# Kernel tuning notes

Hardware: AMD Instinct MI355X
Metric: run time of the kernel (lower is better)

The kernel has to match this reference:

```python
import jax, jax.numpy as jnp
import numpy as np

L, B, F, H, C = 1024, 8, 256, 8, 32  # seq, batch, feature_dim, heads, head_size
EPS = 1e-5


def setup_inputs() -> dict:
    key = jax.random.key(0)
    ks = jax.random.split(key, 12)
    s = 0.02
    f32 = jnp.float32
    return {
        "features": jax.random.normal(ks[0], (L, B, F), f32),
        "ln_g": jnp.ones((F,), f32),
        "ln_b": jnp.zeros((F,), f32),
        "Wq": jax.random.normal(ks[1], (F, H * C), f32) * s,
        "bq": jnp.zeros((H * C,), f32),
        "Wk": jax.random.normal(ks[2], (F, H * C), f32) * s,
        "bk": jnp.zeros((H * C,), f32),
        "Wv": jax.random.normal(ks[3], (F, H * C), f32) * s,
        "bv": jnp.zeros((H * C,), f32),
        "Wb": jax.random.normal(ks[4], (F, H), f32) * s,
        "bb": jnp.zeros((H,), f32),
        "Wg": jax.random.normal(ks[5], (F, H * C), f32) * s,
        "bg": jnp.zeros((H * C,), f32),
        "Wo": jax.random.normal(ks[6], (H * C, F), f32) * s,
        "bo": jnp.zeros((F,), f32),
    }


def _layernorm(x, g, b):
    mu = jnp.mean(x, axis=-1, keepdims=True)
    var = jnp.var(x, axis=-1, keepdims=True)
    return (x - mu) * jax.lax.rsqrt(var + EPS) * g + b


def reference(features, ln_g, ln_b, Wq, bq, Wk, bk, Wv, bv, Wb, bb, Wg, bg, Wo, bo):
    # features: (L, B, F) -- sequence-first layout (see einsum axis analysis)
    x = _layernorm(features, ln_g, ln_b)
    q = (x @ Wq + bq).reshape(L, B, H, C)  # (Lq, B, H, C)
    k = (x @ Wk + bk).reshape(L, B, H, C)  # (Lk, B, H, C)
    v = (x @ Wv + bv).reshape(L, B, H, C)
    bias = x @ Wb + bb                      # (Lk, B, H) per-key-position bias
    gate = jax.nn.sigmoid(x @ Wg + bg).reshape(L, B, H, C)

    sq_c = 1.0 / np.sqrt(C).astype(np.float32)
    # logits[q, b, k, h]
    logits = jnp.einsum('qbhc,kbhc->qbkh', q, k) * sq_c
    logits = logits + jnp.transpose(bias, (1, 0, 2))[None]  # (1, B, Lk, H)
    w = jax.nn.softmax(logits, axis=2)                      # softmax over keys
    attn = jnp.einsum('qbkh,kbhc->qbhc', w, v)              # (Lq, B, H, C)
    out = (attn * gate).reshape(L, B, H * C)
    return out @ Wo + bo                                    # (L, B, F)
```

## Files before the change

kernel.cpp:

```cpp
#include <hip/hip_runtime.h>
#include <math.h>

#define LQ 1024
#define BB 8
#define FF 256
#define HH 8
#define CC 32
#define MROWS (LQ*BB)
static constexpr float EPSV  = 1e-5f;
static constexpr float LOG2E = 1.4426950408889634f;
static constexpr float C1    = 0.17677669529663687f * 1.4426950408889634f;

typedef short  short8  __attribute__((ext_vector_type(8)));
typedef short  short4v __attribute__((ext_vector_type(4)));
typedef float  float4v __attribute__((ext_vector_type(4)));

__device__ inline unsigned short f2bf(float f) {
    unsigned int u = __builtin_bit_cast(unsigned int, f);
    u += 0x7FFFu + ((u >> 16) & 1u);
    return (unsigned short)(u >> 16);
}
__device__ inline float bf2f(unsigned short h) {
    unsigned int u = ((unsigned int)h) << 16;
    return __builtin_bit_cast(float, u);
}
__device__ inline unsigned int cvt_pk_bf16(float a, float b) {
    unsigned int r;
    asm("v_cvt_pk_bf16_f32 %0, %1, %2" : "=v"(r) : "v"(a), "v"(b));
    return r;
}
__device__ __forceinline__ void gl_lds16(const unsigned short* g, unsigned short* l) {
    __builtin_amdgcn_global_load_lds(
        (const __attribute__((address_space(1))) void*)g,
        (__attribute__((address_space(3))) void*)l, 16, 0, 0);
}

__global__ __launch_bounds__(256)
void prep_ln_kernel(const float* __restrict__ x, const float* __restrict__ g,
                    const float* __restrict__ bln,
                    const float* __restrict__ Wq, const float* __restrict__ Wk,
                    const float* __restrict__ Wv, const float* __restrict__ Wg,
                    const float* __restrict__ Wo, const float* __restrict__ Wb,
                    const float* __restrict__ bq, const float* __restrict__ bk,
                    const float* __restrict__ bv, const float* __restrict__ bg,
                    unsigned short* __restrict__ xb, unsigned short* __restrict__ wt,
                    unsigned short* __restrict__ wto,
                    float* __restrict__ bcomb, float* __restrict__ wbt) {
    int bid = blockIdx.x;
    if (bid < 2048) {
        int wid  = threadIdx.x >> 6;
        int lane = threadIdx.x & 63;
        int row  = bid * 4 + wid;
        float4 v = reinterpret_cast<const float4*>(x + (size_t)row * FF)[lane];
        float s  = v.x + v.y + v.z + v.w;
        float sq = v.x*v.x + v.y*v.y + v.z*v.z + v.w*v.w;
        #pragma unroll
        for (int m = 1; m < 64; m <<= 1) {
            s  += __shfl_xor(s,  m);
            sq += __shfl_xor(sq, m);
        }
        float mean = s * (1.0f / FF);
        float var  = sq * (1.0f / FF) - mean * mean;
        float rstd = rsqrtf(var + EPSV);
        float4 gg = reinterpret_cast<const float4*>(g)[lane];
        float4 bv4 = reinterpret_cast<const float4*>(bln)[lane];
        short4v o;
        o[0] = (short)f2bf((v.x - mean) * rstd * gg.x + bv4.x);
        o[1] = (short)f2bf((v.y - mean) * rstd * gg.y + bv4.y);
        o[2] = (short)f2bf((v.z - mean) * rstd * gg.z + bv4.z);
        o[3] = (short)f2bf((v.w - mean) * rstd * gg.w + bv4.w);
        *reinterpret_cast<short4v*>(xb + (size_t)row * FF + lane * 4) = o;
    } else if (bid < 2112) {
        int k0 = (bid - 2048) * 4;
        int nl = threadIdx.x;
        const float* Ws[5] = {Wq, Wk, Wv, Wg, Wo};
        #pragma unroll
        for (int sel = 0; sel < 5; ++sel) {
            const float* W = Ws[sel];
            short4v o;
            #pragma unroll
            for (int j = 0; j < 4; ++j)
                o[j] = (short)f2bf(W[(size_t)(k0 + j) * 256 + nl]);
            unsigned short* dst = (sel < 4)
                ? (wt + ((size_t)sel * 256 + nl) * 256 + k0)
                : (wto + (size_t)nl * 256 + k0);
            *reinterpret_cast<short4v*>(dst) = o;
        }
        if (k0 == 0) {
            bcomb[nl]       = bq[nl];
            bcomb[256 + nl] = bk[nl];
            bcomb[512 + nl] = bv[nl];
            bcomb[768 + nl] = bg[nl];
        }
    } else {
        int nl = threadIdx.x;
        #pragma unroll
        for (int hh = 0; hh < 8; ++hh)
            wbt[hh * 256 + nl] = Wb[(size_t)nl * 8 + hh];
    }
}

__global__ __launch_bounds__(256)
void qkvg_fused_kernel(const unsigned short* __restrict__ A,
                       const unsigned short* __restrict__ Bt,
                       const float* __restrict__ bcomb,
                       const float* __restrict__ wbt,
                       const float* __restrict__ bbv,
                       unsigned short* __restrict__ outq,
                       float* __restrict__ outb) {
    __shared__ unsigned short Asb[128 * 64];
    __shared__ unsigned short Bsb[128 * 64];
    int bid = blockIdx.x;
    int tid = threadIdx.x;

    if (bid >= 512) {
        int idx = (bid - 512) * 256 + tid;
        int row = idx >> 3, hh = idx & 7;
        const unsigned short* xr = A + (size_t)row * 256;
        const float* wr = wbt + hh * 256;
        float s = 0.f;
        #pragma unroll 4
        for (int i = 0; i < 32; ++i) {
            short8 x8 = *reinterpret_cast<const short8*>(xr + i * 8);
            float4 wa = *reinterpret_cast<const float4*>(wr + i * 8);
            float4 wb2 = *reinterpret_cast<const float4*>(wr + i * 8 + 4);
            s += bf2f((unsigned short)x8[0]) * wa.x + bf2f((unsigned short)x8[1]) * wa.y
               + bf2f((unsigned short)x8[2]) * wa.z + bf2f((unsigned short)x8[3]) * wa.w;
            s += bf2f((unsigned short)x8[4]) * wb2.x + bf2f((unsigned short)x8[5]) * wb2.y
               + bf2f((unsigned short)x8[6]) * wb2.z + bf2f((unsigned short)x8[7]) * wb2.w;
        }
        outb[idx] = s + bbv[hh];
        return;
    }

    int lane = tid & 63;
    int w    = tid >> 6;
    int wm   = w >> 1, wn = w & 1;
    int l15  = lane & 15, lg = lane >> 4;
    int bm   = (bid & 63) * 128;
    int bn   = (bid >> 6) * 128;

    float4v acc[4][4];
    #pragma unroll
    for (int i = 0; i < 4; ++i)
        #pragma unroll
        for (int j = 0; j < 4; ++j)
            acc[i][j] = (float4v){0.f, 0.f, 0.f, 0.f};

    for (int k0 = 0; k0 < 256; k0 += 64) {
        __syncthreads();
        #pragma unroll
        for (int j = 0; j < 4; ++j) {
            int c = w * 4 + j;
            int u = c * 64 + lane;
            int row = u >> 3, slot = u & 7;
            size_t gsw = (size_t)row * 256 + k0 + ((slot ^ (row & 7)) * 8);
            gl_lds16(A + (size_t)bm * 256 + gsw, Asb + c * 512);
            gl_lds16(Bt + (size_t)bn * 256 + gsw, Bsb + c * 512);
        }
        __syncthreads();
        #pragma unroll
        for (int kh = 0; kh < 2; ++kh) {
            int slot = kh * 4 + lg;
            short8 af[4], bf[4];
            #pragma unroll
            for (int mf = 0; mf < 4; ++mf) {
                int row = wm * 64 + mf * 16 + l15;
                af[mf] = *reinterpret_cast<const short8*>(
                    Asb + row * 64 + ((slot ^ (row & 7)) * 8));
            }
            #pragma unroll
            for (int nf = 0; nf < 4; ++nf) {
                int row = wn * 64 + nf * 16 + l15;
                bf[nf] = *reinterpret_cast<const short8*>(
                    Bsb + row * 64 + ((slot ^ (row & 7)) * 8));
            }
            #pragma unroll
            for (int mf = 0; mf < 4; ++mf)
                #pragma unroll
                for (int nf = 0; nf < 4; ++nf)
                    acc[mf][nf] = __builtin_amdgcn_mfma_f32_16x16x32_bf16(
                        bf[nf], af[mf], acc[mf][nf], 0, 0, 0);
        }
    }

    int sel = bn >> 8;
    unsigned short* outp = outq + (size_t)sel * MROWS * 256;
    #pragma unroll
    for (int mf = 0; mf < 4; ++mf) {
        int m = bm + wm * 64 + mf * 16 + l15;
        #pragma unroll
        for (int nf = 0; nf < 4; ++nf) {
            int nglob = bn + wn * 64 + nf * 16 + lg * 4;
            float4 b4 = *reinterpret_cast<const float4*>(bcomb + nglob);
            float v0 = acc[mf][nf][0] + b4.x;
            float v1 = acc[mf][nf][1] + b4.y;
            float v2 = acc[mf][nf][2] + b4.z;
            float v3 = acc[mf][nf][3] + b4.w;
            if (sel == 3) {
                v0 = 1.0f / (1.0f + __expf(-v0));
                v1 = 1.0f / (1.0f + __expf(-v1));
                v2 = 1.0f / (1.0f + __expf(-v2));
                v3 = 1.0f / (1.0f + __expf(-v3));
            }
            uint2 st;
            st.x = cvt_pk_bf16(v0, v1);
            st.y = cvt_pk_bf16(v2, v3);
            *reinterpret_cast<uint2*>(outp + (size_t)m * 256 + (nglob & 255)) = st;
        }
    }
}

__global__ __launch_bounds__(512)
void attn_mfma_kernel(const unsigned short* __restrict__ qkvg,
                      const float* __restrict__ biasp,
                      unsigned short* __restrict__ ag) {
    __shared__ unsigned short ksl[128][40];
    __shared__ unsigned short vt[32 * 128];
    __shared__ unsigned short ps[8][16 * 128];
    __shared__ float bias_s[128];
    const unsigned short* qb = qkvg;
    const unsigned short* kb = qkvg + (size_t)MROWS * 256;
    const unsigned short* vb = qkvg + (size_t)MROWS * 256 * 2;
    const unsigned short* gb = qkvg + (size_t)MROWS * 256 * 3;

    int tid  = threadIdx.x;
    int lane = tid & 63;
    int w    = tid >> 6;
    int l15  = lane & 15, lg = lane >> 4;
    int bh   = blockIdx.y;
    int b    = bh >> 3, h = bh & 7;
    int qrow0 = blockIdx.x * 128 + w * 16;

    int krow = tid >> 2, kc8 = (tid & 3) * 8;
    int cv = (tid & 7) * 4, kp = tid >> 3;

    short8 qf = *reinterpret_cast<const short8*>(
        qb + ((size_t)(qrow0 + l15) * 8 + b) * 256 + h * 32 + lg * 8);

    float lsum = 0.f;
    float4v oacc0 = {0.f, 0.f, 0.f, 0.f}, oacc1 = {0.f, 0.f, 0.f, 0.f};

    short8 kreg; short4v v0r, v1r; float breg = 0.f;
    {
        kreg = *reinterpret_cast<const short8*>(
            kb + ((size_t)krow * 8 + b) * 256 + h * 32 + kc8);
        const unsigned short* vp =
            vb + ((size_t)(2 * kp) * 8 + b) * 256 + h * 32 + cv;
        v0r = *reinterpret_cast<const short4v*>(vp);
        v1r = *reinterpret_cast<const short4v*>(vp + 8 * 256);
        if (tid < 128) breg = biasp[(size_t)tid * 64 + b * 8 + h] * LOG2E;
    }

    for (int c0 = 0; c0 < LQ; c0 += 128) {
        __syncthreads();
        *reinterpret_cast<short8*>(&ksl[krow][kc8]) = kreg;
        #pragma unroll
        for (int j = 0; j < 4; ++j) {
            int c = cv + j;
            unsigned int pk = (unsigned int)(unsigned short)v0r[j] |
                              ((unsigned int)(unsigned short)v1r[j] << 16);
            int slot = kp >> 2;
            int off  = c * 128 + ((slot ^ (c & 7)) * 8) + ((2 * kp) & 7);
            *reinterpret_cast<unsigned int*>(&vt[off]) = pk;
        }
        if (tid < 128) bias_s[tid] = breg;
        __syncthreads();
        int cn = c0 + 128;
        if (cn < LQ) {
            kreg = *reinterpret_cast<const short8*>(
                kb + ((size_t)(cn + krow) * 8 + b) * 256 + h * 32 + kc8);
            const unsigned short* vp =
                vb + ((size_t)(cn + 2 * kp) * 8 + b) * 256 + h * 32 + cv;
            v0r = *reinterpret_cast<const short4v*>(vp);
            v1r = *reinterpret_cast<const short4v*>(vp + 8 * 256);
            if (tid < 128) breg = biasp[(size_t)(cn + tid) * 64 + b * 8 + h] * LOG2E;
        }

        __builtin_amdgcn_s_setprio(1);
        float4v sc[8];
        #pragma unroll
        for (int kt = 0; kt < 8; ++kt) {
            short8 kf = *reinterpret_cast<const short8*>(&ksl[kt * 16 + l15][lg * 8]);
            sc[kt] = __builtin_amdgcn_mfma_f32_16x16x32_bf16(
                kf, qf, (float4v){0.f, 0.f, 0.f, 0.f}, 0, 0, 0);
        }
        __builtin_amdgcn_s_setprio(0);

        float psum = 0.f;
        #pragma unroll
        for (int kt = 0; kt < 8; ++kt) {
            float4v b4 = *reinterpret_cast<const float4v*>(&bias_s[kt * 16 + lg * 4]);
            float p0 = __builtin_amdgcn_exp2f(fmaf(sc[kt][0], C1, b4[0]));
            float p1 = __builtin_amdgcn_exp2f(fmaf(sc[kt][1], C1, b4[1]));
            float p2 = __builtin_amdgcn_exp2f(fmaf(sc[kt][2], C1, b4[2]));
            float p3 = __builtin_amdgcn_exp2f(fmaf(sc[kt][3], C1, b4[3]));
            psum += (p0 + p1) + (p2 + p3);
            uint2 pk;
            pk.x = cvt_pk_bf16(p0, p1);
            pk.y = cvt_pk_bf16(p2, p3);
            int slot = kt * 2 + (lg >> 1);
            int off  = l15 * 128 + ((slot ^ (l15 & 7)) * 8) + (lg & 1) * 4;
            *reinterpret_cast<uint2*>(&ps[w][off]) = pk;
        }
        psum += __shfl_xor(psum, 16);
        psum += __shfl_xor(psum, 32);
        lsum += psum;

        __builtin_amdgcn_s_setprio(1);
        #pragma unroll
        for (int kh = 0; kh < 4; ++kh) {
            int slot = kh * 4 + lg;
            short8 pf = *reinterpret_cast<const short8*>(
                &ps[w][l15 * 128 + ((slot ^ (l15 & 7)) * 8)]);
            int c0r = l15, c1r = 16 + l15;
            short8 vf0 = *reinterpret_cast<const short8*>(
                &vt[c0r * 128 + ((slot ^ (c0r & 7)) * 8)]);
            short8 vf1 = *reinterpret_cast<const short8*>(
                &vt[c1r * 128 + ((slot ^ (c1r & 7)) * 8)]);
            oacc0 = __builtin_amdgcn_mfma_f32_16x16x32_bf16(vf0, pf, oacc0, 0, 0, 0);
            oacc1 = __builtin_amdgcn_mfma_f32_16x16x32_bf16(vf1, pf, oacc1, 0, 0, 0);
        }
        __builtin_amdgcn_s_setprio(0);
    }

    float linv = 1.0f / lsum;
    size_t base = ((size_t)(qrow0 + l15) * 8 + b) * 256 + h * 32;
    #pragma unroll
    for (int ct = 0; ct < 2; ++ct) {
        int c0 = ct * 16 + lg * 4;
        float4v oa = ct ? oacc1 : oacc0;
        short4v g4 = *reinterpret_cast<const short4v*>(gb + base + c0);
        float v0 = oa[0] * linv * bf2f((unsigned short)g4[0]);
        float v1 = oa[1] * linv * bf2f((unsigned short)g4[1]);
        float v2 = oa[2] * linv * bf2f((unsigned short)g4[2]);
        float v3 = oa[3] * linv * bf2f((unsigned short)g4[3]);
        uint2 st;
        st.x = cvt_pk_bf16(v0, v1);
        st.y = cvt_pk_bf16(v2, v3);
        *reinterpret_cast<uint2*>(ag + base + c0) = st;
    }
}

__global__ __launch_bounds__(256)
void gemm_out_kernel(const unsigned short* __restrict__ A,
                     const unsigned short* __restrict__ Bt,
                     const float* __restrict__ bias,
                     float* __restrict__ Cout) {
    __shared__ unsigned short Asb[64 * 64];
    __shared__ unsigned short Bsb[128 * 64];
    int tid  = threadIdx.x;
    int lane = tid & 63;
    int w    = tid >> 6;
    int l15  = lane & 15, lg = lane >> 4;
    int bm   = blockIdx.x * 64;
    int bn   = blockIdx.y * 128;

    float4v acc[4][2];
    #pragma unroll
    for (int i = 0; i < 4; ++i)
        #pragma unroll
        for (int j = 0; j < 2; ++j)
            acc[i][j] = (float4v){0.f, 0.f, 0.f, 0.f};

    for (int k0 = 0; k0 < 256; k0 += 64) {
        __syncthreads();
        #pragma unroll
        for (int j = 0; j < 2; ++j) {
            int c = w * 2 + j;
            int u = c * 64 + lane;
            int row = u >> 3, slot = u & 7;
            gl_lds16(A + (size_t)(bm + row) * 256 + k0 + ((slot ^ (row & 7)) * 8),
                     Asb + c * 512);
        }
        #pragma unroll
        for (int j = 0; j < 4; ++j) {
            int c = w * 4 + j;
            int u = c * 64 + lane;
            int row = u >> 3, slot = u & 7;
            gl_lds16(Bt + (size_t)(bn + row) * 256 + k0 + ((slot ^ (row & 7)) * 8),
                     Bsb + c * 512);
        }
        __syncthreads();
        #pragma unroll
        for (int kh = 0; kh < 2; ++kh) {
            int slot = kh * 4 + lg;
            short8 af[4], bf[2];
            #pragma unroll
            for (int mf = 0; mf < 4; ++mf) {
                int row = mf * 16 + l15;
                af[mf] = *reinterpret_cast<const short8*>(
                    Asb + row * 64 + ((slot ^ (row & 7)) * 8));
            }
            #pragma unroll
            for (int nf = 0; nf < 2; ++nf) {
                int row = w * 32 + nf * 16 + l15;
                bf[nf] = *reinterpret_cast<const short8*>(
                    Bsb + row * 64 + ((slot ^ (row & 7)) * 8));
            }
            #pragma unroll
            for (int mf = 0; mf < 4; ++mf)
                #pragma unroll
                for (int nf = 0; nf < 2; ++nf)
                    acc[mf][nf] = __builtin_amdgcn_mfma_f32_16x16x32_bf16(
                        bf[nf], af[mf], acc[mf][nf], 0, 0, 0);
        }
    }
    #pragma unroll
    for (int mf = 0; mf < 4; ++mf) {
        int m = bm + mf * 16 + l15;
        #pragma unroll
        for (int nf = 0; nf < 2; ++nf) {
            int c0 = bn + w * 32 + nf * 16 + lg * 4;
            float4 b4 = *reinterpret_cast<const float4*>(bias + c0);
            float4 o;
            o.x = acc[mf][nf][0] + b4.x;
            o.y = acc[mf][nf][1] + b4.y;
            o.z = acc[mf][nf][2] + b4.z;
            o.w = acc[mf][nf][3] + b4.w;
            *reinterpret_cast<float4*>(Cout + (size_t)m * 256 + c0) = o;
        }
    }
}

extern "C" void kernel_launch(void* const* d_in, const int* in_sizes, int n_in,
                              void* d_out, int out_size, void* d_ws, size_t ws_size,
                              hipStream_t stream) {
    (void)in_sizes; (void)n_in; (void)out_size; (void)ws_size;
    const float* features = (const float*)d_in[0];
    const float* ln_g = (const float*)d_in[1];
    const float* ln_b = (const float*)d_in[2];
    const float* Wq = (const float*)d_in[3];
    const float* bq = (const float*)d_in[4];
    const float* Wk = (const float*)d_in[5];
    const float* bk = (const float*)d_in[6];
    const float* Wv = (const float*)d_in[7];
    const float* bv = (const float*)d_in[8];
    const float* Wb = (const float*)d_in[9];
    const float* bbv = (const float*)d_in[10];
    const float* Wg = (const float*)d_in[11];
    const float* bg = (const float*)d_in[12];
    const float* Wo = (const float*)d_in[13];
    const float* bo = (const float*)d_in[14];
    float* out = (float*)d_out;

    char* wsb = (char*)d_ws;
    unsigned short* xb    = (unsigned short*)(wsb);
    unsigned short* wt    = (unsigned short*)(wsb + 4194304);
    unsigned short* wto   = (unsigned short*)(wsb + 4718592);
    float*          bcomb = (float*)(wsb + 4849664);
    float*          wbt   = (float*)(wsb + 4853760);
    unsigned short* qkvg  = (unsigned short*)(wsb + 4861952);
    float*          biasb = (float*)(wsb + 21639168);
    unsigned short* agb   = (unsigned short*)(wsb + 21901312);

    prep_ln_kernel<<<dim3(2113), dim3(256), 0, stream>>>(
        features, ln_g, ln_b, Wq, Wk, Wv, Wg, Wo, Wb,
        bq, bk, bv, bg, xb, wt, wto, bcomb, wbt);
    qkvg_fused_kernel<<<dim3(768), dim3(256), 0, stream>>>(
        xb, wt, bcomb, wbt, bbv, qkvg, biasb);
    attn_mfma_kernel<<<dim3(8, 64), dim3(512), 0, stream>>>(
        qkvg, biasb, agb);
    gemm_out_kernel<<<dim3(128, 2), dim3(256), 0, stream>>>(
        agb, wto, bo, out);
}
```

Baseline: 59.38 us.

## Give each attention wave two query tiles and halve the block size

The attention kernel now runs 4 waves per block instead of 8, and each wave handles 32 query rows (two 16-row MFMA tiles). Each K and V fragment read from LDS is reused across both query tiles. Each 128-key chunk is split into two 64-key halves so the per-wave P scratch buffer stays small. The aim is fewer LDS reads per MFMA and less block-wide staging overhead, at the cost of more registers per thread and fewer waves available to hide latency.

```diff
diff --git a/kernel.cpp b/kernel.cpp
--- a/kernel.cpp
+++ b/kernel.cpp
@@ -211,13 +211,13 @@
     }
 }
 
-__global__ __launch_bounds__(512)
+__global__ __launch_bounds__(256)
 void attn_mfma_kernel(const unsigned short* __restrict__ qkvg,
                       const float* __restrict__ biasp,
                       unsigned short* __restrict__ ag) {
     __shared__ unsigned short ksl[128][40];
     __shared__ unsigned short vt[32 * 128];
-    __shared__ unsigned short ps[8][16 * 128];
+    __shared__ unsigned short ps[4][32 * 64];
     __shared__ float bias_s[128];
     const unsigned short* qb = qkvg;
     const unsigned short* kb = qkvg + (size_t)MROWS * 256;
@@ -230,115 +230,172 @@
     int l15  = lane & 15, lg = lane >> 4;
     int bh   = blockIdx.y;
     int b    = bh >> 3, h = bh & 7;
-    int qrow0 = blockIdx.x * 128 + w * 16;
-
-    int krow = tid >> 2, kc8 = (tid & 3) * 8;
-    int cv = (tid & 7) * 4, kp = tid >> 3;
-
-    short8 qf = *reinterpret_cast<const short8*>(
-        qb + ((size_t)(qrow0 + l15) * 8 + b) * 256 + h * 32 + lg * 8);
-
-    float lsum = 0.f;
-    float4v oacc0 = {0.f, 0.f, 0.f, 0.f}, oacc1 = {0.f, 0.f, 0.f, 0.f};
-
-    short8 kreg; short4v v0r, v1r; float breg = 0.f;
+    int qrow0 = blockIdx.x * 128 + w * 32;
+
+    int cv = (tid & 7) * 4, kp0 = tid >> 3;
+
+    short8 qf[2];
+    #pragma unroll
+    for (int qt = 0; qt < 2; ++qt)
+        qf[qt] = *reinterpret_cast<const short8*>(
+            qb + ((size_t)(qrow0 + qt * 16 + l15) * 8 + b) * 256 + h * 32 + lg * 8);
+
+    float lsum[2] = {0.f, 0.f};
+    float4v oacc[2][2];
+    #pragma unroll
+    for (int i = 0; i < 2; ++i)
+        #pragma unroll
+        for (int j = 0; j < 2; ++j) oacc[i][j] = (float4v){0.f, 0.f, 0.f, 0.f};
+
+    short8 kreg[2]; short4v v0r[2], v1r[2]; float breg = 0.f;
     {
-        kreg = *reinterpret_cast<const short8*>(
-            kb + ((size_t)krow * 8 + b) * 256 + h * 32 + kc8);
-        const unsigned short* vp =
-            vb + ((size_t)(2 * kp) * 8 + b) * 256 + h * 32 + cv;
-        v0r = *reinterpret_cast<const short4v*>(vp);
-        v1r = *reinterpret_cast<const short4v*>(vp + 8 * 256);
+        #pragma unroll
+        for (int j = 0; j < 2; ++j) {
+            int u = j * 256 + tid;
+            int row = u >> 2, slot = u & 3;
+            kreg[j] = *reinterpret_cast<const short8*>(
+                kb + ((size_t)row * 8 + b) * 256 + h * 32 + slot * 8);
+        }
+        #pragma unroll
+        for (int gI = 0; gI < 2; ++gI) {
+            const unsigned short* vp =
+                vb + ((size_t)(2 * kp0 + 64 * gI) * 8 + b) * 256 + h * 32 + cv;
+            v0r[gI] = *reinterpret_cast<const short4v*>(vp);
+            v1r[gI] = *reinterpret_cast<const short4v*>(vp + 8 * 256);
+        }
         if (tid < 128) breg = biasp[(size_t)tid * 64 + b * 8 + h] * LOG2E;
     }
 
     for (int c0 = 0; c0 < LQ; c0 += 128) {
         __syncthreads();
-        *reinterpret_cast<short8*>(&ksl[krow][kc8]) = kreg;
-        #pragma unroll
-        for (int j = 0; j < 4; ++j) {
-            int c = cv + j;
-            unsigned int pk = (unsigned int)(unsigned short)v0r[j] |
-                              ((unsigned int)(unsigned short)v1r[j] << 16);
+        #pragma unroll
+        for (int j = 0; j < 2; ++j) {
+            int u = j * 256 + tid;
+            int row = u >> 2, slot = u & 3;
+            *reinterpret_cast<short8*>(&ksl[row][slot * 8]) = kreg[j];
+        }
+        #pragma unroll
+        for (int gI = 0; gI < 2; ++gI) {
+            int kp = kp0 + 32 * gI;
             int slot = kp >> 2;
-            int off  = c * 128 + ((slot ^ (c & 7)) * 8) + ((2 * kp) & 7);
-            *reinterpret_cast<unsigned int*>(&vt[off]) = pk;
+            #pragma unroll
+            for (int j = 0; j < 4; ++j) {
+                int c = cv + j;
+                unsigned int pk = (unsigned int)(unsigned short)v0r[gI][j] |
+                                  ((unsigned int)(unsigned short)v1r[gI][j] << 16);
+                int off = c * 128 + ((slot ^ (c & 7)) * 8) + ((2 * kp0) & 7);
+                *reinterpret_cast<unsigned int*>(&vt[off]) = pk;
+            }
         }
         if (tid < 128) bias_s[tid] = breg;
         __syncthreads();
         int cn = c0 + 128;
         if (cn < LQ) {
-            kreg = *reinterpret_cast<const short8*>(
-                kb + ((size_t)(cn + krow) * 8 + b) * 256 + h * 32 + kc8);
-            const unsigned short* vp =
-                vb + ((size_t)(cn + 2 * kp) * 8 + b) * 256 + h * 32 + cv;
-            v0r = *reinterpret_cast<const short4v*>(vp);
-            v1r = *reinterpret_cast<const short4v*>(vp + 8 * 256);
+            #pragma unroll
+            for (int j = 0; j < 2; ++j) {
+                int u = j * 256 + tid;
+                int row = u >> 2, slot = u & 3;
+                kreg[j] = *reinterpret_cast<const short8*>(
+                    kb + ((size_t)(cn + row) * 8 + b) * 256 + h * 32 + slot * 8);
+            }
+            #pragma unroll
+            for (int gI = 0; gI < 2; ++gI) {
+                const unsigned short* vp =
+                    vb + ((size_t)(cn + 2 * kp0 + 64 * gI) * 8 + b) * 256 + h * 32 + cv;
+                v0r[gI] = *reinterpret_cast<const short4v*>(vp);
+                v1r[gI] = *reinterpret_cast<const short4v*>(vp + 8 * 256);
+            }
             if (tid < 128) breg = biasp[(size_t)(cn + tid) * 64 + b * 8 + h] * LOG2E;
         }
 
-        __builtin_amdgcn_s_setprio(1);
-        float4v sc[8];
-        #pragma unroll
-        for (int kt = 0; kt < 8; ++kt) {
-            short8 kf = *reinterpret_cast<const short8*>(&ksl[kt * 16 + l15][lg * 8]);
-            sc[kt] = __builtin_amdgcn_mfma_f32_16x16x32_bf16(
-                kf, qf, (float4v){0.f, 0.f, 0.f, 0.f}, 0, 0, 0);
-        }
-        __builtin_amdgcn_s_setprio(0);
-
-        float psum = 0.f;
-        #pragma unroll
-        for (int kt = 0; kt < 8; ++kt) {
-            float4v b4 = *reinterpret_cast<const float4v*>(&bias_s[kt * 16 + lg * 4]);
-            float p0 = __builtin_amdgcn_exp2f(fmaf(sc[kt][0], C1, b4[0]));
-            float p1 = __builtin_amdgcn_exp2f(fmaf(sc[kt][1], C1, b4[1]));
-            float p2 = __builtin_amdgcn_exp2f(fmaf(sc[kt][2], C1, b4[2]));
-            float p3 = __builtin_amdgcn_exp2f(fmaf(sc[kt][3], C1, b4[3]));
-            psum += (p0 + p1) + (p2 + p3);
-            uint2 pk;
-            pk.x = cvt_pk_bf16(p0, p1);
-            pk.y = cvt_pk_bf16(p2, p3);
-            int slot = kt * 2 + (lg >> 1);
-            int off  = l15 * 128 + ((slot ^ (l15 & 7)) * 8) + (lg & 1) * 4;
-            *reinterpret_cast<uint2*>(&ps[w][off]) = pk;
-        }
-        psum += __shfl_xor(psum, 16);
-        psum += __shfl_xor(psum, 32);
-        lsum += psum;
-
-        __builtin_amdgcn_s_setprio(1);
-        #pragma unroll
-        for (int kh = 0; kh < 4; ++kh) {
-            int slot = kh * 4 + lg;
-            short8 pf = *reinterpret_cast<const short8*>(
-                &ps[w][l15 * 128 + ((slot ^ (l15 & 7)) * 8)]);
-            int c0r = l15, c1r = 16 + l15;
-            short8 vf0 = *reinterpret_cast<const short8*>(
-                &vt[c0r * 128 + ((slot ^ (c0r & 7)) * 8)]);
-            short8 vf1 = *reinterpret_cast<const short8*>(
-                &vt[c1r * 128 + ((slot ^ (c1r & 7)) * 8)]);
-            oacc0 = __builtin_amdgcn_mfma_f32_16x16x32_bf16(vf0, pf, oacc0, 0, 0, 0);
-            oacc1 = __builtin_amdgcn_mfma_f32_16x16x32_bf16(vf1, pf, oacc1, 0, 0, 0);
-        }
-        __builtin_amdgcn_s_setprio(0);
-    }
-
-    float linv = 1.0f / lsum;
-    size_t base = ((size_t)(qrow0 + l15) * 8 + b) * 256 + h * 32;
-    #pragma unroll
-    for (int ct = 0; ct < 2; ++ct) {
-        int c0 = ct * 16 + lg * 4;
-        float4v oa = ct ? oacc1 : oacc0;
-        short4v g4 = *reinterpret_cast<const short4v*>(gb + base + c0);
-        float v0 = oa[0] * linv * bf2f((unsigned short)g4[0]);
-        float v1 = oa[1] * linv * bf2f((unsigned short)g4[1]);
-        float v2 = oa[2] * linv * bf2f((unsigned short)g4[2]);
-        float v3 = oa[3] * linv * bf2f((unsigned short)g4[3]);
-        uint2 st;
-        st.x = cvt_pk_bf16(v0, v1);
-        st.y = cvt_pk_bf16(v2, v3);
-        *reinterpret_cast<uint2*>(ag + base + c0) = st;
+        #pragma unroll
+        for (int half = 0; half < 2; ++half) {
+            __builtin_amdgcn_s_setprio(1);
+            float4v sc[2][4];
+            #pragma unroll
+            for (int kt = 0; kt < 4; ++kt) {
+                short8 kf = *reinterpret_cast<const short8*>(
+                    &ksl[half * 64 + kt * 16 + l15][lg * 8]);
+                #pragma unroll
+                for (int qt = 0; qt < 2; ++qt)
+                    sc[qt][kt] = __builtin_amdgcn_mfma_f32_16x16x32_bf16(
+                        kf, qf[qt], (float4v){0.f, 0.f, 0.f, 0.f}, 0, 0, 0);
+            }
+            __builtin_amdgcn_s_setprio(0);
+
+            #pragma unroll
+            for (int qt = 0; qt < 2; ++qt) {
+                int prow = qt * 16 + l15;
+                unsigned short* pw = &ps[w][prow * 64];
+                int rsw = prow & 7;
+                float psum = 0.f;
+                #pragma unroll
+                for (int kt = 0; kt < 4; ++kt) {
+                    float4v b4 = *reinterpret_cast<const float4v*>(
+                        &bias_s[half * 64 + kt * 16 + lg * 4]);
+                    float p0 = __builtin_amdgcn_exp2f(fmaf(sc[qt][kt][0], C1, b4[0]));
+                    float p1 = __builtin_amdgcn_exp2f(fmaf(sc[qt][kt][1], C1, b4[1]));
+                    float p2 = __builtin_amdgcn_exp2f(fmaf(sc[qt][kt][2], C1, b4[2]));
+                    float p3 = __builtin_amdgcn_exp2f(fmaf(sc[qt][kt][3], C1, b4[3]));
+                    psum += (p0 + p1) + (p2 + p3);
+                    uint2 pk;
+                    pk.x = cvt_pk_bf16(p0, p1);
+                    pk.y = cvt_pk_bf16(p2, p3);
+                    int slot = kt * 2 + (lg >> 1);
+                    *reinterpret_cast<uint2*>(
+                        &pw[((slot ^ rsw) * 8) + (lg & 1) * 4]) = pk;
+                }
+                psum += __shfl_xor(psum, 16);
+                psum += __shfl_xor(psum, 32);
+                lsum[qt] += psum;
+            }
+
+            __builtin_amdgcn_s_setprio(1);
+            #pragma unroll
+            for (int sub = 0; sub < 2; ++sub) {
+                int pslot = sub * 4 + lg;
+                int vslot = (half * 2 + sub) * 4 + lg;
+                short8 pf[2], vf[2];
+                #pragma unroll
+                for (int qt = 0; qt < 2; ++qt) {
+                    int prow = qt * 16 + l15;
+                    pf[qt] = *reinterpret_cast<const short8*>(
+                        &ps[w][prow * 64 + ((pslot ^ (prow & 7)) * 8)]);
+                }
+                #pragma unroll
+                for (int ct = 0; ct < 2; ++ct) {
+                    int crow = ct * 16 + l15;
+                    vf[ct] = *reinterpret_cast<const short8*>(
+                        &vt[crow * 128 + ((vslot ^ (crow & 7)) * 8)]);
+                }
+                #pragma unroll
+                for (int qt = 0; qt < 2; ++qt)
+                    #pragma unroll
+                    for (int ct = 0; ct < 2; ++ct)
+                        oacc[qt][ct] = __builtin_amdgcn_mfma_f32_16x16x32_bf16(
+                            vf[ct], pf[qt], oacc[qt][ct], 0, 0, 0);
+            }
+            __builtin_amdgcn_s_setprio(0);
+        }
+    }
+
+    #pragma unroll
+    for (int qt = 0; qt < 2; ++qt) {
+        float linv = 1.0f / lsum[qt];
+        size_t base = ((size_t)(qrow0 + qt * 16 + l15) * 8 + b) * 256 + h * 32;
+        #pragma unroll
+        for (int ct = 0; ct < 2; ++ct) {
+            int cc0 = ct * 16 + lg * 4;
+            short4v g4 = *reinterpret_cast<const short4v*>(gb + base + cc0);
+            float v0 = oacc[qt][ct][0] * linv * bf2f((unsigned short)g4[0]);
+            float v1 = oacc[qt][ct][1] * linv * bf2f((unsigned short)g4[1]);
+            float v2 = oacc[qt][ct][2] * linv * bf2f((unsigned short)g4[2]);
+            float v3 = oacc[qt][ct][3] * linv * bf2f((unsigned short)g4[3]);
+            uint2 st;
+            st.x = cvt_pk_bf16(v0, v1);
+            st.y = cvt_pk_bf16(v2, v3);
+            *reinterpret_cast<uint2*>(ag + base + cc0) = st;
+        }
     }
 }
 
@@ -459,7 +516,7 @@
         bq, bk, bv, bg, xb, wt, wto, bcomb, wbt);
     qkvg_fused_kernel<<<dim3(768), dim3(256), 0, stream>>>(
         xb, wt, bcomb, wbt, bbv, qkvg, biasb);
-    attn_mfma_kernel<<<dim3(8, 64), dim3(512), 0, stream>>>(
+    attn_mfma_kernel<<<dim3(8, 64), dim3(256), 0, stream>>>(
         qkvg, biasb, agb);
     gemm_out_kernel<<<dim3(128, 2), dim3(256), 0, stream>>>(
         agb, wto, bo, out);
```

After: 63.63 us. 1.07x slower.
